# Optimization experiments

Measured on AMD Instinct MI355X. Metric: run time of the kernel, lower is better.

## Reference

```python
import jax, jax.numpy as jnp
import numpy as np

# RSC encoder from gen_poly = ('101', '111'): feedback poly g0 = 1 + D^2, parity poly g1 = 1 + D + D^2
G0 = (1, 0, 1)
G1 = (1, 1, 1)
MU = 2  # constraint_length - 1
B, K = 2048, 6144


def _xor(a, b):
    # GF(2) XOR expressed on {0,1} floats: a + b - 2ab (exact on bits, differentiable)
    return a + b - 2.0 * a * b


def _rsc_encode(u):
    """Recursive systematic convolutional encoding.

    u: [B, k] float bits. Returns parity bits [B, k].
    State recursion (per time step):
      fb      = u_t XOR sum_{i: g0[i+1]=1} state[i]
      parity  = g1[0]*fb XOR sum_{i: g1[i+1]=1} state[i]
      state   = [fb, state[:-1]]
    """
    def step(state, ut):  # state: [B, MU], ut: [B]
        fb = ut
        for i in range(MU):
            if G0[i + 1]:
                fb = _xor(fb, state[:, i])
        par = fb if G1[0] else jnp.zeros_like(fb)
        for i in range(MU):
            if G1[i + 1]:
                par = _xor(par, state[:, i])
        new_state = jnp.concatenate([fb[:, None], state[:, :-1]], axis=1)
        return new_state, par

    init = jnp.zeros((u.shape[0], MU), u.dtype)
    _, par = jax.lax.scan(step, init, u.T)  # scan over time axis -> par: [k, B]
    return par.T


def setup_inputs() -> dict:
    key = jax.random.key(0)
    k1, k2 = jax.random.split(key)
    bits = jax.random.randint(k1, (B, K), 0, 2).astype(jnp.float32)
    perm = jax.random.permutation(k2, K).astype(jnp.int32)  # fixed interleaver permutation
    return {"bits": bits, "perm": perm}


def reference(bits, perm):
    # Encoder 1 on the systematic bits, encoder 2 on the interleaved bits.
    p1 = _rsc_encode(bits)
    p2 = _rsc_encode(bits[:, perm])
    # Rate-1/3 Turbo codeword: per time step [sys, parity1, parity2]
    cw = jnp.stack([bits, p1, p2], axis=-1).reshape(bits.shape[0], 3 * bits.shape[1])
    return cw.astype(jnp.float32)
```

## Files before the change

### kernel.cpp

```cpp
#include <hip/hip_runtime.h>
#include <stdint.h>

#define KLEN  6144
#define BROWS 2048
#define NG    (BROWS / 32)
#define GK    (NG * KLEN)
#define NT    256

#define NT2   512
#define CL2   (KLEN / NT2)

#define ET    768
#define NTILE (KLEN / ET)
#define EMIT_GRID (NG * NTILE)
#define QROW  (3 * ET / 4)
#define QPB   (32 * QROW)

typedef float vfloat4 __attribute__((ext_vector_type(4)));


__global__ __launch_bounds__(NT) void pack_kernel(const float* __restrict__ bits,
                                                  uint32_t* __restrict__ packedS) {
    int task = blockIdx.x * NT + threadIdx.x;
    int g  = task / (KLEN / 4);
    int tq = task - g * (KLEN / 4);
    const float* rb = bits + (size_t)g * 32 * KLEN + 4 * tq;
    uint32_t w0 = 0, w1 = 0, w2 = 0, w3 = 0;
#pragma unroll 1
    for (int j0 = 0; j0 < 32; j0 += 8) {
#pragma unroll
        for (int j = 0; j < 8; ++j) {
            float4 f = *(const float4*)(rb + (size_t)(j0 + j) * KLEN);
            w0 |= (f.x > 0.5f ? 1u : 0u) << (j0 + j);
            w1 |= (f.y > 0.5f ? 1u : 0u) << (j0 + j);
            w2 |= (f.z > 0.5f ? 1u : 0u) << (j0 + j);
            w3 |= (f.w > 0.5f ? 1u : 0u) << (j0 + j);
        }
    }
    *(uint4*)(packedS + g * KLEN + 4 * tq) = make_uint4(w0, w1, w2, w3);
}

__global__ __launch_bounds__(NT2) void scan_kernel(const uint32_t* __restrict__ packedS,
                                                   const int* __restrict__ perm,
                                                   uint32_t* __restrict__ p1,
                                                   uint32_t* __restrict__ p2) {
    __shared__ uint32_t a0[NT2], a1[NT2];
    int c   = threadIdx.x;
    int enc = blockIdx.x >> 6;
    int g   = blockIdx.x & (NG - 1);
    const uint32_t* base = packedS + g * KLEN;
    int t0 = c * CL2;

    uint32_t u[CL2];
    if (enc) {
#pragma unroll
        for (int i = 0; i < CL2; ++i) u[i] = base[perm[t0 + i]];
    } else {
#pragma unroll
        for (int i = 0; i < CL2; ++i) u[i] = base[t0 + i];
    }

    uint32_t s0 = 0, s1 = 0;
#pragma unroll
    for (int i = 0; i < CL2; ++i) { uint32_t n0 = u[i] ^ s1; s1 = s0; s0 = n0; }

    a0[c] = s0; a1[c] = s1;
    __syncthreads();
#pragma unroll
    for (int off = 1; off < NT2; off <<= 1) {
        uint32_t x0 = 0, x1 = 0;
        if (c >= off) { x0 = a0[c - off]; x1 = a1[c - off]; }
        __syncthreads();
        a0[c] ^= x0; a1[c] ^= x1;
        __syncthreads();
    }
    s0 = c ? a0[c - 1] : 0u;
    s1 = c ? a1[c - 1] : 0u;

    uint32_t* __restrict__ pout = enc ? p2 : p1;
    uint32_t pq0, pq1, pq2;
#pragma unroll
    for (int i = 0; i < CL2; ++i) {
        uint32_t pv = u[i] ^ s0;
        uint32_t n0 = u[i] ^ s1; s1 = s0; s0 = n0;
        if ((i & 3) == 0) pq0 = pv;
        else if ((i & 3) == 1) pq1 = pv;
        else if ((i & 3) == 2) pq2 = pv;
        else *(uint4*)(pout + g * KLEN + t0 + i - 3) = make_uint4(pq0, pq1, pq2, pv);
    }
}

__global__ __launch_bounds__(NT) void emit_kernel(const uint32_t* __restrict__ ps,
                                                  const uint32_t* __restrict__ p1,
                                                  const uint32_t* __restrict__ p2,
                                                  float* __restrict__ out) {
    __shared__ uint32_t l0[ET], l1[ET], l2[ET];
    int blk  = blockIdx.x;
    int g    = blk / NTILE;
    int tile = blk - g * NTILE;
    int i    = threadIdx.x;

    size_t pbase = (size_t)g * KLEN + (size_t)tile * ET;
    if (i < ET / 4) {
        *(uint4*)(l0 + 4 * i) = *(const uint4*)(ps + pbase + 4 * i);
        *(uint4*)(l1 + 4 * i) = *(const uint4*)(p1 + pbase + 4 * i);
        *(uint4*)(l2 + 4 * i) = *(const uint4*)(p2 + pbase + 4 * i);
    }
    __syncthreads();

    float* gout = out + (size_t)(g * 32) * (3 * KLEN) + (size_t)tile * (3 * ET);
#pragma unroll 2
    for (int k = 0; k < QPB / NT; ++k) {
        int idx  = k * NT + i;
        int row  = idx / QROW;
        int qq   = idx - row * QROW;
        int pos0 = 4 * qq;
        int t0   = pos0 / 3;
        int r0   = pos0 - 3 * t0;
        uint32_t w00 = l0[t0],     w01 = l1[t0],     w02 = l2[t0];
        uint32_t w10 = l0[t0 + 1], w11 = l1[t0 + 1], w12 = l2[t0 + 1];
        uint32_t e0 = r0 == 0 ? w00 : (r0 == 1 ? w01 : w02);
        uint32_t e1 = r0 == 0 ? w01 : (r0 == 1 ? w02 : w10);
        uint32_t e2 = r0 == 0 ? w02 : (r0 == 1 ? w10 : w11);
        uint32_t e3 = r0 == 0 ? w10 : (r0 == 1 ? w11 : w12);
        int bit = row;
        vfloat4 f;
        f.x = (float)((e0 >> bit) & 1u);
        f.y = (float)((e1 >> bit) & 1u);
        f.z = (float)((e2 >> bit) & 1u);
        f.w = (float)((e3 >> bit) & 1u);
        __builtin_nontemporal_store(f,
            (vfloat4*)(gout + (size_t)row * (3 * KLEN) + pos0));
    }
}

extern "C" void kernel_launch(void* const* d_in, const int* in_sizes, int n_in,
                              void* d_out, int out_size, void* d_ws, size_t ws_size,
                              hipStream_t stream) {
    const float* bits = (const float*)d_in[0];
    const int*   perm = (const int*)d_in[1];
    float* out = (float*)d_out;

    uint32_t* ws = (uint32_t*)d_ws;
    uint32_t* packedS = ws;
    uint32_t* p1      = ws + (size_t)GK;
    uint32_t* p2      = ws + (size_t)2 * GK;

    hipLaunchKernelGGL(pack_kernel, dim3(GK / 4 / NT), dim3(NT), 0, stream,
                       bits, packedS);
    hipLaunchKernelGGL(scan_kernel, dim3(2 * NG), dim3(NT2), 0, stream,
                       packedS, perm, p1, p2);
    hipLaunchKernelGGL(emit_kernel, dim3(EMIT_GRID), dim3(NT), 0, stream,
                       packedS, p1, p2, out);
}
```

Before: 53.02 us.

## Compute parity inside emit kernel from per-tile scan carries

The scan kernel now only produces the carry state at each 768-step tile boundary, using 256 threads with 24 steps each, and no longer writes full p1/p2 parity arrays. The emit kernel recomputes the parity for its own tile with a block-level XOR prefix scan over 384 threads covering pairs of steps, seeded by those carries. This removes the global write and read of both parity arrays and shrinks the middle kernel. In exchange each emit block does extra gather loads through perm and a 9-step shared-memory scan with many barriers.

```diff
diff --git a/kernel.cpp b/kernel.cpp
--- a/kernel.cpp
+++ b/kernel.cpp
@@ -7,13 +7,13 @@
 #define GK    (NG * KLEN)
 #define NT    256
 
-#define NT2   512
-#define CL2   (KLEN / NT2)
+#define CLE   24
 
-#define ET    768
-#define NTILE (KLEN / ET)
+#define ET3   768
+#define NTILE (KLEN / ET3)
+#define NT3   384
 #define EMIT_GRID (NG * NTILE)
-#define QROW  (3 * ET / 4)
+#define QROW  (3 * ET3 / 4)
 #define QPB   (32 * QROW)
 
 typedef float vfloat4 __attribute__((ext_vector_type(4)));
@@ -40,78 +40,97 @@
     *(uint4*)(packedS + g * KLEN + 4 * tq) = make_uint4(w0, w1, w2, w3);
 }
 
-__global__ __launch_bounds__(NT2) void scan_kernel(const uint32_t* __restrict__ packedS,
-                                                   const int* __restrict__ perm,
-                                                   uint32_t* __restrict__ p1,
-                                                   uint32_t* __restrict__ p2) {
-    __shared__ uint32_t a0[NT2], a1[NT2];
+__global__ __launch_bounds__(NT) void ends_kernel(const uint32_t* __restrict__ packedS,
+                                                  const int* __restrict__ perm,
+                                                  uint32_t* __restrict__ ends) {
+    __shared__ uint32_t a0[NT], a1[NT];
     int c   = threadIdx.x;
     int enc = blockIdx.x >> 6;
     int g   = blockIdx.x & (NG - 1);
     const uint32_t* base = packedS + g * KLEN;
-    int t0 = c * CL2;
+    int t0 = c * CLE;
 
-    uint32_t u[CL2];
+    uint32_t s0 = 0, s1 = 0;
     if (enc) {
 #pragma unroll
-        for (int i = 0; i < CL2; ++i) u[i] = base[perm[t0 + i]];
+        for (int i = 0; i < CLE; ++i) {
+            uint32_t u = base[perm[t0 + i]];
+            uint32_t n0 = u ^ s1; s1 = s0; s0 = n0;
+        }
     } else {
 #pragma unroll
-        for (int i = 0; i < CL2; ++i) u[i] = base[t0 + i];
+        for (int i = 0; i < CLE; ++i) {
+            uint32_t u = base[t0 + i];
+            uint32_t n0 = u ^ s1; s1 = s0; s0 = n0;
+        }
     }
-
-    uint32_t s0 = 0, s1 = 0;
-#pragma unroll
-    for (int i = 0; i < CL2; ++i) { uint32_t n0 = u[i] ^ s1; s1 = s0; s0 = n0; }
 
     a0[c] = s0; a1[c] = s1;
     __syncthreads();
 #pragma unroll
-    for (int off = 1; off < NT2; off <<= 1) {
+    for (int off = 1; off < NT; off <<= 1) {
         uint32_t x0 = 0, x1 = 0;
         if (c >= off) { x0 = a0[c - off]; x1 = a1[c - off]; }
         __syncthreads();
         a0[c] ^= x0; a1[c] ^= x1;
         __syncthreads();
     }
-    s0 = c ? a0[c - 1] : 0u;
-    s1 = c ? a1[c - 1] : 0u;
-
-    uint32_t* __restrict__ pout = enc ? p2 : p1;
-    uint32_t pq0, pq1, pq2;
-#pragma unroll
-    for (int i = 0; i < CL2; ++i) {
-        uint32_t pv = u[i] ^ s0;
-        uint32_t n0 = u[i] ^ s1; s1 = s0; s0 = n0;
-        if ((i & 3) == 0) pq0 = pv;
-        else if ((i & 3) == 1) pq1 = pv;
-        else if ((i & 3) == 2) pq2 = pv;
-        else *(uint4*)(pout + g * KLEN + t0 + i - 3) = make_uint4(pq0, pq1, pq2, pv);
+    if ((c & 31) == 0) {
+        int tile = c >> 5;
+        int idx = ((enc * NG + g) * NTILE + tile) * 2;
+        ends[idx + 0] = c ? a0[c - 1] : 0u;
+        ends[idx + 1] = c ? a1[c - 1] : 0u;
     }
 }
 
-__global__ __launch_bounds__(NT) void emit_kernel(const uint32_t* __restrict__ ps,
-                                                  const uint32_t* __restrict__ p1,
-                                                  const uint32_t* __restrict__ p2,
-                                                  float* __restrict__ out) {
-    __shared__ uint32_t l0[ET], l1[ET], l2[ET];
-    int blk  = blockIdx.x;
-    int g    = blk / NTILE;
-    int tile = blk - g * NTILE;
+__global__ __launch_bounds__(NT3) void emit_kernel(const uint32_t* __restrict__ packedS,
+                                                   const int* __restrict__ perm,
+                                                   const uint32_t* __restrict__ ends,
+                                                   float* __restrict__ out) {
+    __shared__ uint32_t l0[ET3], l1[ET3], l2[ET3];
+    __shared__ uint32_t c0[NT3], c1[NT3], d0[NT3], d1[NT3];
     int i    = threadIdx.x;
+    int g    = blockIdx.x / NTILE;
+    int tile = blockIdx.x - g * NTILE;
+    const uint32_t* base = packedS + g * KLEN;
+    int tb = tile * ET3;
+    int ta = tb + 2 * i;
 
-    size_t pbase = (size_t)g * KLEN + (size_t)tile * ET;
-    if (i < ET / 4) {
-        *(uint4*)(l0 + 4 * i) = *(const uint4*)(ps + pbase + 4 * i);
-        *(uint4*)(l1 + 4 * i) = *(const uint4*)(p1 + pbase + 4 * i);
-        *(uint4*)(l2 + 4 * i) = *(const uint4*)(p2 + pbase + 4 * i);
+    uint32_t ua = base[ta], ub = base[ta + 1];
+    uint32_t va = base[perm[ta]], vb = base[perm[ta + 1]];
+    l0[2 * i] = ua; l0[2 * i + 1] = ub;
+
+    c0[i] = ub; c1[i] = ua; d0[i] = vb; d1[i] = va;
+    __syncthreads();
+#pragma unroll
+    for (int off = 1; off < NT3; off <<= 1) {
+        uint32_t x0 = 0, x1 = 0, y0 = 0, y1 = 0;
+        if (i >= off) { x0 = c0[i - off]; x1 = c1[i - off];
+                        y0 = d0[i - off]; y1 = d1[i - off]; }
+        __syncthreads();
+        c0[i] ^= x0; c1[i] ^= x1; d0[i] ^= y0; d1[i] ^= y1;
+        __syncthreads();
     }
+
+    int eidx = (g * NTILE + tile) * 2;
+    int fidx = ((NG + g) * NTILE + tile) * 2;
+    uint32_t s0 = (i ? c0[i - 1] : 0u) ^ ends[eidx + 0];
+    uint32_t s1 = (i ? c1[i - 1] : 0u) ^ ends[eidx + 1];
+    uint32_t q0 = (i ? d0[i - 1] : 0u) ^ ends[fidx + 0];
+    uint32_t q1 = (i ? d1[i - 1] : 0u) ^ ends[fidx + 1];
+
+    uint32_t p1a = ua ^ s0;
+    uint32_t p1b = ub ^ (ua ^ s1);
+    uint32_t p2a = va ^ q0;
+    uint32_t p2b = vb ^ (va ^ q1);
+    l1[2 * i] = p1a; l1[2 * i + 1] = p1b;
+    l2[2 * i] = p2a; l2[2 * i + 1] = p2b;
     __syncthreads();
 
-    float* gout = out + (size_t)(g * 32) * (3 * KLEN) + (size_t)tile * (3 * ET);
+    float* gout = out + (size_t)(g * 32) * (3 * KLEN) + (size_t)tile * (3 * ET3);
 #pragma unroll 2
-    for (int k = 0; k < QPB / NT; ++k) {
-        int idx  = k * NT + i;
+    for (int k = 0; k < QPB / NT3; ++k) {
+        int idx  = k * NT3 + i;
         int row  = idx / QROW;
         int qq   = idx - row * QROW;
         int pos0 = 4 * qq;
@@ -143,13 +162,12 @@
 
     uint32_t* ws = (uint32_t*)d_ws;
     uint32_t* packedS = ws;
-    uint32_t* p1      = ws + (size_t)GK;
-    uint32_t* p2      = ws + (size_t)2 * GK;
+    uint32_t* ends    = ws + (size_t)GK;
 
     hipLaunchKernelGGL(pack_kernel, dim3(GK / 4 / NT), dim3(NT), 0, stream,
                        bits, packedS);
-    hipLaunchKernelGGL(scan_kernel, dim3(2 * NG), dim3(NT2), 0, stream,
-                       packedS, perm, p1, p2);
-    hipLaunchKernelGGL(emit_kernel, dim3(EMIT_GRID), dim3(NT), 0, stream,
-                       packedS, p1, p2, out);
+    hipLaunchKernelGGL(ends_kernel, dim3(2 * NG), dim3(NT), 0, stream,
+                       packedS, perm, ends);
+    hipLaunchKernelGGL(emit_kernel, dim3(EMIT_GRID), dim3(NT3), 0, stream,
+                       packedS, perm, ends, out);
 }
```

Measured after the change: 55.17 us. +4.1%, slower.
